# Kernel tuning notes

Measured on AMD Instinct MI355X. Metric: run time of the kernel, lower is better.

Reference implementation:

```python
import jax, jax.numpy as jnp
import numpy as np

INPUT_DIM = 128
DEPTH = 6
HIDDEN = 64
NUM_INNER = 2 ** DEPTH - 1  # 63
NUM_LEAVES = 2 ** DEPTH     # 64


def setup_inputs() -> dict:
    key = jax.random.key(0)
    ks = jax.random.split(key, 6)
    x = jax.random.normal(ks[0], (65536, INPUT_DIM), dtype=jnp.float32)
    s1 = 1.0 / np.sqrt(INPUT_DIM)
    s2 = 1.0 / np.sqrt(HIDDEN)
    W1 = jax.random.uniform(ks[1], (NUM_INNER, INPUT_DIM, HIDDEN), minval=-s1, maxval=s1, dtype=jnp.float32)
    b1 = jax.random.uniform(ks[2], (NUM_INNER, HIDDEN), minval=-s1, maxval=s1, dtype=jnp.float32)
    W2 = jax.random.uniform(ks[3], (NUM_INNER, HIDDEN), minval=-s2, maxval=s2, dtype=jnp.float32)
    b2 = jax.random.uniform(ks[4], (NUM_INNER,), minval=-s2, maxval=s2, dtype=jnp.float32)
    leaf = jax.random.normal(ks[5], (NUM_LEAVES, 1), dtype=jnp.float32)
    return {"x": x, "W1": W1, "b1": b1, "W2": W2, "b2": b2, "leaf": leaf}


def reference(x, W1, b1, W2, b2, leaf):
    # All inner-node MLPs as one batched GEMM pair: [B, N] node probabilities
    h = jax.nn.relu(jnp.einsum('bi,nih->bnh', x, W1) + b1)      # [B, N, H]
    probs = jax.nn.sigmoid(jnp.einsum('bnh,nh->bn', h, W2) + b2)  # [B, N]

    # Original code walks node_idx = 2*node_idx+1 unconditionally, so the chain
    # of used node indices is 2^k - 1 for k = 0..depth-1.
    chain = jnp.array([2 ** k - 1 for k in range(DEPTH)], dtype=jnp.int32)
    p_chain = probs[:, chain]  # [B, D]

    # Bit k (LSB first) of leaf index selects p (bit=1) vs 1-p (bit=0)
    leaves = np.arange(NUM_LEAVES)
    bits = jnp.asarray(((leaves[:, None] >> np.arange(DEPTH)[None, :]) & 1).astype(np.float32))  # [L, D]

    # path_probs[b, l] = prod_k ( bits[l,k]*p + (1-bits[l,k])*(1-p) )
    factors = bits[None, :, :] * p_chain[:, None, :] + (1.0 - bits[None, :, :]) * (1.0 - p_chain[:, None, :])  # [B, L, D]
    path_probs = jnp.prod(factors, axis=-1)  # [B, L]

    return (path_probs @ leaf)[:, 0]  # [B]
```

## Files before the change

### kernel.cpp

```cpp
#include <hip/hip_runtime.h>

typedef __attribute__((ext_vector_type(4))) float f32x4;
typedef __attribute__((ext_vector_type(8))) short bf16x8;

#define IDIM   128
#define HID    64
#define TDEPTH 6
#define MTILE  64
#define NWAVES 6
#define BLOCK  (NWAVES * 64)
#define WFRAG_ELEMS (6 * 4 * 4 * 512)

__device__ __forceinline__ unsigned short f2bf(float f) {
    unsigned int u = __builtin_bit_cast(unsigned int, f);
    unsigned int r = (u + 0x7FFFu + ((u >> 16) & 1u)) >> 16;
    return (unsigned short)r;
}

__global__ void prep_wfrag(const float* __restrict__ W1, unsigned short* __restrict__ wfrag) {
    int idx = blockIdx.x * 256 + threadIdx.x;
    if (idx >= WFRAG_ELEMS) return;
    int j    = idx & 7;
    int lane = (idx >> 3) & 63;
    int ct   = (idx >> 9) & 3;
    int ks   = (idx >> 11) & 3;
    int nd   = idx >> 13;
    int node = (1 << nd) - 1;
    int k    = ks * 32 + (lane >> 4) * 8 + j;
    int col  = ct * 16 + (lane & 15);
    wfrag[idx] = f2bf(W1[(node * IDIM + k) * HID + col]);
}

template <bool USE_WS>
__global__ __launch_bounds__(BLOCK, 3)
void sdt_kernel(const float* __restrict__ x, const float* __restrict__ W1,
                const float* __restrict__ b1, const float* __restrict__ W2,
                const float* __restrict__ b2, const float* __restrict__ leaf,
                const unsigned short* __restrict__ wfrag, float* __restrict__ out) {
    __shared__ unsigned short xs[MTILE][IDIM + 8];
    __shared__ float p_lds[TDEPTH][MTILE];

    const int tid    = threadIdx.x;
    const int m_base = blockIdx.x * MTILE;

    const float4* xv = reinterpret_cast<const float4*>(x) + (size_t)m_base * (IDIM / 4);
    for (int f = tid; f < MTILE * (IDIM / 4); f += BLOCK) {
        int row = f >> 5;
        int c4  = f & 31;
        float4 v = xv[row * 32 + c4];
        unsigned long long pk =
            (unsigned long long)f2bf(v.x) |
            ((unsigned long long)f2bf(v.y) << 16) |
            ((unsigned long long)f2bf(v.z) << 32) |
            ((unsigned long long)f2bf(v.w) << 48);
        *reinterpret_cast<unsigned long long*>(&xs[row][c4 * 4]) = pk;
    }
    __syncthreads();

    const int wave = tid >> 6;
    const int lane = tid & 63;
    const int node = (1 << wave) - 1;
    const int lcol = lane & 15;
    const int lq   = lane >> 4;

    f32x4 acc[4][4];
    #pragma unroll
    for (int rt = 0; rt < 4; rt++)
        #pragma unroll
        for (int ct = 0; ct < 4; ct++)
            acc[rt][ct] = (f32x4){0.f, 0.f, 0.f, 0.f};

    #pragma unroll
    for (int ks = 0; ks < 4; ks++) {
        bf16x8 bfrag[4];
        if (USE_WS) {
            #pragma unroll
            for (int ct = 0; ct < 4; ct++)
                bfrag[ct] = *reinterpret_cast<const bf16x8*>(
                    wfrag + (((wave * 4 + ks) * 4 + ct) * 512 + lane * 8));
        } else {
            const float* wsrc = W1 + (size_t)node * IDIM * HID;
            int k0 = ks * 32 + lq * 8;
            #pragma unroll
            for (int ct = 0; ct < 4; ct++) {
                int col = ct * 16 + lcol;
                bf16x8 v;
                #pragma unroll
                for (int j = 0; j < 8; j++)
                    v[j] = (short)f2bf(wsrc[(k0 + j) * HID + col]);
                bfrag[ct] = v;
            }
        }
        bf16x8 afrag[4];
        #pragma unroll
        for (int rt = 0; rt < 4; rt++)
            afrag[rt] = *reinterpret_cast<const bf16x8*>(&xs[rt * 16 + lcol][ks * 32 + lq * 8]);
        #pragma unroll
        for (int rt = 0; rt < 4; rt++)
            #pragma unroll
            for (int ct = 0; ct < 4; ct++)
                acc[rt][ct] = __builtin_amdgcn_mfma_f32_16x16x32_bf16(
                    afrag[rt], bfrag[ct], acc[rt][ct], 0, 0, 0);
    }

    float b1v[4], w2v[4];
    #pragma unroll
    for (int ct = 0; ct < 4; ct++) {
        int col = ct * 16 + lcol;
        b1v[ct] = b1[node * HID + col];
        w2v[ct] = W2[node * HID + col];
    }
    const float bias2 = b2[node];
    #pragma unroll
    for (int rt = 0; rt < 4; rt++) {
        #pragma unroll
        for (int r = 0; r < 4; r++) {
            float s = 0.f;
            #pragma unroll
            for (int ct = 0; ct < 4; ct++) {
                float v = acc[rt][ct][r] + b1v[ct];
                v = v > 0.f ? v : 0.f;
                s += v * w2v[ct];
            }
            #pragma unroll
            for (int d = 1; d < 16; d <<= 1)
                s += __shfl_xor(s, d, 64);
            float p = 1.f / (1.f + __expf(-(s + bias2)));
            if (lcol == 0)
                p_lds[wave][rt * 16 + lq * 4 + r] = p;
        }
    }
    __syncthreads();

    if (tid < MTILE) {
        float pk[TDEPTH];
        #pragma unroll
        for (int k = 0; k < TDEPTH; k++) pk[k] = p_lds[k][tid];
        float o = 0.f;
        for (int l = 0; l < 64; l++) {
            float w = leaf[l];
            #pragma unroll
            for (int k = 0; k < TDEPTH; k++)
                w *= ((l >> k) & 1) ? pk[k] : (1.f - pk[k]);
            o += w;
        }
        out[m_base + tid] = o;
    }
}

extern "C" void kernel_launch(void* const* d_in, const int* in_sizes, int n_in,
                              void* d_out, int out_size, void* d_ws, size_t ws_size,
                              hipStream_t stream) {
    const float* x    = (const float*)d_in[0];
    const float* W1   = (const float*)d_in[1];
    const float* b1   = (const float*)d_in[2];
    const float* W2   = (const float*)d_in[3];
    const float* b2   = (const float*)d_in[4];
    const float* leaf = (const float*)d_in[5];
    float* out = (float*)d_out;

    const int Bn = in_sizes[0] / IDIM;
    const int nblocks = Bn / MTILE;

    if (ws_size >= (size_t)WFRAG_ELEMS * sizeof(unsigned short)) {
        unsigned short* wfrag = (unsigned short*)d_ws;
        prep_wfrag<<<(WFRAG_ELEMS + 255) / 256, 256, 0, stream>>>(W1, wfrag);
        sdt_kernel<true><<<nblocks, BLOCK, 0, stream>>>(x, W1, b1, W2, b2, leaf, wfrag, out);
    } else {
        sdt_kernel<false><<<nblocks, BLOCK, 0, stream>>>(x, W1, b1, W2, b2, leaf, nullptr, out);
    }
}
```

Measured before the change: 108.0 us.

## Factor leaf reduction into lerp tree split across four waves; hoist bias loads

Measured after the change: 107.7 us. About the same (-0.3%).

```diff
diff --git a/kernel.cpp b/kernel.cpp
--- a/kernel.cpp
+++ b/kernel.cpp
@@ -39,6 +39,7 @@
                 const unsigned short* __restrict__ wfrag, float* __restrict__ out) {
     __shared__ unsigned short xs[MTILE][IDIM + 8];
     __shared__ float p_lds[TDEPTH][MTILE];
+    __shared__ float pp[4][MTILE];
 
     const int tid    = threadIdx.x;
     const int m_base = blockIdx.x * MTILE;
@@ -55,13 +56,23 @@
             ((unsigned long long)f2bf(v.w) << 48);
         *reinterpret_cast<unsigned long long*>(&xs[row][c4 * 4]) = pk;
     }
-    __syncthreads();
 
     const int wave = tid >> 6;
     const int lane = tid & 63;
     const int node = (1 << wave) - 1;
     const int lcol = lane & 15;
     const int lq   = lane >> 4;
+
+    float b1v[4], w2v[4];
+    #pragma unroll
+    for (int ct = 0; ct < 4; ct++) {
+        int col = ct * 16 + lcol;
+        b1v[ct] = b1[node * HID + col];
+        w2v[ct] = W2[node * HID + col];
+    }
+    const float bias2 = b2[node];
+
+    __syncthreads();
 
     f32x4 acc[4][4];
     #pragma unroll
@@ -103,14 +114,6 @@
                     afrag[rt], bfrag[ct], acc[rt][ct], 0, 0, 0);
     }
 
-    float b1v[4], w2v[4];
-    #pragma unroll
-    for (int ct = 0; ct < 4; ct++) {
-        int col = ct * 16 + lcol;
-        b1v[ct] = b1[node * HID + col];
-        w2v[ct] = W2[node * HID + col];
-    }
-    const float bias2 = b2[node];
     #pragma unroll
     for (int rt = 0; rt < 4; rt++) {
         #pragma unroll
@@ -132,20 +135,34 @@
     }
     __syncthreads();
 
-    if (tid < MTILE) {
-        float pk[TDEPTH];
+    if (tid < 4 * MTILE) {
+        int row = tid & (MTILE - 1);
+        int ch  = tid >> 6;
+        float q0 = p_lds[0][row];
+        float q1 = p_lds[1][row];
+        float q2 = p_lds[2][row];
+        float q3 = p_lds[3][row];
+        float p4 = p_lds[4][row];
+        float p5 = p_lds[5][row];
+        float f4 = (ch & 1) ? p4 : 1.f - p4;
+        float f5 = (ch & 2) ? p5 : 1.f - p5;
+        const float* lf = leaf + ch * 16;
+        float t[8];
         #pragma unroll
-        for (int k = 0; k < TDEPTH; k++) pk[k] = p_lds[k][tid];
-        float o = 0.f;
-        for (int l = 0; l < 64; l++) {
-            float w = leaf[l];
-            #pragma unroll
-            for (int k = 0; k < TDEPTH; k++)
-                w *= ((l >> k) & 1) ? pk[k] : (1.f - pk[k]);
-            o += w;
+        for (int j = 0; j < 8; j++) {
+            float a = lf[2 * j], b = lf[2 * j + 1];
+            t[j] = a + q0 * (b - a);
         }
-        out[m_base + tid] = o;
+        #pragma unroll
+        for (int j = 0; j < 4; j++) t[j] = t[2 * j] + q1 * (t[2 * j + 1] - t[2 * j]);
+        #pragma unroll
+        for (int j = 0; j < 2; j++) t[j] = t[2 * j] + q2 * (t[2 * j + 1] - t[2 * j]);
+        float s = t[0] + q3 * (t[1] - t[0]);
+        pp[ch][row] = f4 * f5 * s;
     }
+    __syncthreads();
+    if (tid < MTILE)
+        out[m_base + tid] = (pp[0][tid] + pp[1][tid]) + (pp[2][tid] + pp[3][tid]);
 }
 
 extern "C" void kernel_launch(void* const* d_in, const int* in_sizes, int n_in,
```
